# Kernel tuning notes

Measured on AMD Instinct MI355X. Metric: run time of the kernel, lower is better.

Reference implementation:

```python
import jax, jax.numpy as jnp
import numpy as np

B, H, W, C, NH, WS, SS = 32, 56, 56, 192, 6, 7, 3
L = H * W
N = WS * WS
HD = C // NH
EPS = 1e-3  # keras LayerNormalization default epsilon


def _rel_index(ws):
    coords = np.stack(np.meshgrid(np.arange(ws), np.arange(ws), indexing='ij')).reshape(2, -1)
    rel = (coords[:, :, None] - coords[:, None, :]).transpose(1, 2, 0)
    rel[..., 0] += ws - 1
    rel[..., 1] += ws - 1
    rel[..., 0] *= 2 * ws - 1
    return rel.sum(-1)  # (N, N) int


def _attn_mask(h, w, ws, ss):
    img = np.zeros((h, w), np.float32)
    cnt = 0
    for hs in (slice(0, -ws), slice(-ws, -ss), slice(-ss, None)):
        for wsl in (slice(0, -ws), slice(-ws, -ss), slice(-ss, None)):
            img[hs, wsl] = cnt
            cnt += 1
    mw = img.reshape(h // ws, ws, w // ws, ws).transpose(0, 2, 1, 3).reshape(-1, ws * ws)
    diff = mw[:, None, :] - mw[:, :, None]  # expand_dims(mw,1) - expand_dims(mw,2)
    return np.where(diff != 0, -100.0, 0.0).astype(np.float32)  # (nW, N, N)


REL_IDX = _rel_index(WS)
ATTN_MASK = _attn_mask(H, W, WS, SS)


def _ln(x, g, b):
    m = x.mean(-1, keepdims=True)
    v = x.var(-1, keepdims=True)
    return (x - m) / jnp.sqrt(v + EPS) * g + b


def setup_inputs() -> dict:
    key = jax.random.key(0)
    ks = jax.random.split(key, 8)
    s = 0.02
    return {
        'x': jax.random.normal(ks[0], (B, L, C), jnp.float32),
        'gamma1': jnp.ones((C,), jnp.float32),
        'beta1': jnp.zeros((C,), jnp.float32),
        'qkv_w': jax.random.normal(ks[1], (C, 3 * C), jnp.float32) * s,
        'qkv_b': jnp.zeros((3 * C,), jnp.float32),
        'proj_w': jax.random.normal(ks[2], (C, C), jnp.float32) * s,
        'proj_b': jnp.zeros((C,), jnp.float32),
        'rel_bias_table': jax.random.normal(ks[3], ((2 * WS - 1) ** 2, NH), jnp.float32) * s,
        'gamma2': jnp.ones((C,), jnp.float32),
        'beta2': jnp.zeros((C,), jnp.float32),
        'fc1_w': jax.random.normal(ks[4], (C, 4 * C), jnp.float32) * s,
        'fc1_b': jnp.zeros((4 * C,), jnp.float32),
        'fc2_w': jax.random.normal(ks[5], (4 * C, C), jnp.float32) * s,
        'fc2_b': jnp.zeros((C,), jnp.float32),
    }


def reference(x, gamma1, beta1, qkv_w, qkv_b, proj_w, proj_b, rel_bias_table,
              gamma2, beta2, fc1_w, fc1_b, fc2_w, fc2_b):
    scale = HD ** -0.5
    shortcut = x
    # norm1 + cyclic shift + window partition
    xn = _ln(x, gamma1, beta1).reshape(B, H, W, C)
    xn = jnp.roll(xn, (-SS, -SS), axis=(1, 2))
    xw = xn.reshape(B, H // WS, WS, W // WS, WS, C).transpose(0, 1, 3, 2, 4, 5).reshape(-1, N, C)
    # window attention
    qkv = (xw @ qkv_w + qkv_b).reshape(-1, N, 3, NH, HD).transpose(2, 0, 3, 1, 4)
    q, k, v = qkv[0] * scale, qkv[1], qkv[2]  # (B*nW, NH, N, HD)
    attn = jnp.einsum('whnd,whmd->whnm', q, k)
    bias = rel_bias_table[REL_IDX.reshape(-1)].reshape(N, N, NH).transpose(2, 0, 1)
    attn = attn + bias[None]
    nW = ATTN_MASK.shape[0]
    attn = attn.reshape(B, nW, NH, N, N) + jnp.asarray(ATTN_MASK)[None, :, None]
    attn = jax.nn.softmax(attn.reshape(-1, NH, N, N), axis=-1)
    out = jnp.einsum('whnm,whmd->whnd', attn, v).transpose(0, 2, 1, 3).reshape(-1, N, C)
    out = out @ proj_w + proj_b
    # window reverse + reverse shift
    xr = out.reshape(B, H // WS, W // WS, WS, WS, C).transpose(0, 1, 3, 2, 4, 5).reshape(B, H, W, C)
    xr = jnp.roll(xr, (SS, SS), axis=(1, 2)).reshape(B, L, C)
    x = shortcut + xr
    # MLP block
    y = _ln(x, gamma2, beta2)
    y = jax.nn.gelu(y @ fc1_w + fc1_b, approximate=False) @ fc2_w + fc2_b
    return x + y
```

## Files before the change

kernel.cpp:

```cpp
#include <hip/hip_runtime.h>
#include <math.h>

namespace {
constexpr int kBatch = 32, kH = 56, kW = 56, kC = 192, kNH = 6, kWS = 7, kSS = 3;
constexpr int kL   = kH * kW;
constexpr int kN   = kWS * kWS;
constexpr int kTok = kBatch * kL;
constexpr int kNWin = kTok / kN;
constexpr float kEps   = 1e-3f;
constexpr float kScale = 0.17677669529663687f;
}

typedef unsigned short u16;
typedef __attribute__((ext_vector_type(8))) short short8;
typedef __attribute__((ext_vector_type(4))) float f32x4;

__device__ __forceinline__ float bf2f(u16 u) {
    return __uint_as_float(((unsigned int)u) << 16);
}
__device__ __forceinline__ u16 f2bf(float f) {
    unsigned int x = __float_as_uint(f);
    return (u16)((x + 0x7FFFu + ((x >> 16) & 1u)) >> 16);
}
__device__ __forceinline__ float gelu_f(float x) {
    float z = 0.7978845608028654f * x * (1.0f + 0.044715f * x * x);
    float t = 1.0f - 2.0f / (1.0f + __expf(2.0f * z));
    return 0.5f * x * (1.0f + t);
}

__global__ __launch_bounds__(256) void ln_kernel(
    const float* __restrict__ x, const float* __restrict__ gamma,
    const float* __restrict__ beta, u16* __restrict__ out, int do_shift)
{
    const int wave = threadIdx.x >> 6;
    const int lane = threadIdx.x & 63;
    const int tok = (blockIdx.x << 2) + wave;
    const float* xp = x + (size_t)tok * kC;
    float v0 = xp[lane], v1 = xp[lane + 64], v2 = xp[lane + 128];
    float s  = v0 + v1 + v2;
    float sq = v0 * v0 + v1 * v1 + v2 * v2;
    #pragma unroll
    for (int off = 32; off > 0; off >>= 1) {
        s  += __shfl_down(s, off, 64);
        sq += __shfl_down(sq, off, 64);
    }
    s  = __shfl(s, 0, 64);
    sq = __shfl(sq, 0, 64);
    const float mean = s * (1.0f / kC);
    const float var  = sq * (1.0f / kC) - mean * mean;
    const float inv  = rsqrtf(var + kEps);
    size_t orow;
    if (do_shift) {
        const int b = tok / kL, hw = tok % kL;
        const int h = hw / kW, w = hw % kW;
        const int hs = (h + kH - kSS) % kH;
        const int ws = (w + kW - kSS) % kW;
        const int wh = hs / kWS, ii = hs % kWS;
        const int ww = ws / kWS, jj = ws % kWS;
        orow = (size_t)(b * 64 + wh * 8 + ww) * kN + (ii * kWS + jj);
    } else {
        orow = tok;
    }
    u16* op = out + orow * kC;
    op[lane]       = f2bf((v0 - mean) * inv * gamma[lane]       + beta[lane]);
    op[lane + 64]  = f2bf((v1 - mean) * inv * gamma[lane + 64]  + beta[lane + 64]);
    op[lane + 128] = f2bf((v2 - mean) * inv * gamma[lane + 128] + beta[lane + 128]);
}

__global__ __launch_bounds__(256) void wprep_qkv(
    const float* __restrict__ w, u16* __restrict__ wt)
{
    const int idx = blockIdx.x * 256 + threadIdx.x;
    if (idx >= 576 * 192) return;
    const int n = idx / 192, k = idx - n * 192;
    float v = w[(size_t)k * 576 + n];
    if (n < 192) v *= kScale;
    wt[idx] = f2bf(v);
}

__global__ __launch_bounds__(256) void wprep_rest(
    const float* __restrict__ pw, const float* __restrict__ f1w,
    const float* __restrict__ f2w, u16* __restrict__ proj_t,
    u16* __restrict__ f1_t, u16* __restrict__ f2_t)
{
    int idx = blockIdx.x * 256 + threadIdx.x;
    if (idx < 36864) {
        const int n = idx / 192, k = idx - n * 192;
        proj_t[idx] = f2bf(pw[(size_t)k * 192 + n]);
        return;
    }
    idx -= 36864;
    if (idx < 147456) {
        const int n = idx / 192, k = idx - n * 192;
        f1_t[idx] = f2bf(f1w[(size_t)k * 768 + n]);
        return;
    }
    idx -= 147456;
    if (idx < 147456) {
        const int n = idx / 768, k = idx - n * 768;
        f2_t[idx] = f2bf(f2w[(size_t)k * 192 + n]);
    }
}

__global__ __launch_bounds__(256) void prep_bm(
    const float* __restrict__ btab, const float* __restrict__ qkv_b,
    float* __restrict__ T, float* __restrict__ qkv_bs)
{
    const int idx = blockIdx.x * 256 + threadIdx.x;
    if (idx < 576) qkv_bs[idx] = (idx < 192) ? qkv_b[idx] * kScale : qkv_b[idx];
    if (idx >= 4 * 6 * 49 * 49) return;
    const int m = idx % 49, n = (idx / 49) % 49;
    const int head = (idx / 2401) % 6, cls = idx / (2401 * 6);
    const int i1 = n / 7, j1 = n % 7, i2 = m / 7, j2 = m % 7;
    float v = btab[((i1 - i2 + 6) * 13 + (j1 - j2 + 6)) * kNH + head];
    const int whE = cls >> 1, wwE = cls & 1;
    const int r1 = (whE ? (i1 < 4 ? 1 : 2) : 0) * 3 + (wwE ? (j1 < 4 ? 1 : 2) : 0);
    const int r2 = (whE ? (i2 < 4 ? 1 : 2) : 0) * 3 + (wwE ? (j2 < 4 ? 1 : 2) : 0);
    if (r1 != r2) v -= 100.f;
    T[idx] = v;
}

template <int MODE, int K, int NJ>
__global__ __launch_bounds__(256) void gemm_mfma(
    const u16* __restrict__ A, const u16* __restrict__ Bt, int ldb,
    const float* __restrict__ bias, const float* __restrict__ aux,
    void* __restrict__ outv, u16* __restrict__ vt = nullptr)
{
    constexpr int Nn = NJ * 192;
    constexpr int Kp = K + 8;
    __shared__ u16 As[64 * Kp];
    const int tid  = threadIdx.x;
    const int wave = tid >> 6, lane = tid & 63;
    const int quad = lane >> 4, l15 = lane & 15;
    const int m0 = blockIdx.x * 64;

    {
        const u16* src = A + (size_t)m0 * K;
        #pragma unroll
        for (int i = tid; i < 64 * K / 8; i += 256) {
            const int e = i * 8;
            const int r = e / K, c = e - r * K;
            *(short8*)&As[r * Kp + c] = *(const short8*)(src + e);
        }
    }
    __syncthreads();

    #pragma unroll
    for (int j = 0; j < NJ; ++j) {
        const int nb0 = j * 192 + wave * 48;
        const u16* Bbase = Bt + (size_t)(nb0 + l15) * ldb + quad * 8;
        f32x4 acc[4][3] = {};
        #pragma unroll
        for (int ks = 0; ks < K / 32; ++ks) {
            short8 a[4], b[3];
            #pragma unroll
            for (int i = 0; i < 4; ++i)
                a[i] = *(const short8*)&As[(i * 16 + l15) * Kp + ks * 32 + quad * 8];
            #pragma unroll
            for (int t = 0; t < 3; ++t)
                b[t] = *(const short8*)(Bbase + (size_t)t * 16 * ldb + ks * 32);
            #pragma unroll
            for (int i = 0; i < 4; ++i)
                #pragma unroll
                for (int t = 0; t < 3; ++t)
                    acc[i][t] = __builtin_amdgcn_mfma_f32_16x16x32_bf16(
                        a[i], b[t], acc[i][t], 0, 0, 0);
        }
        float bcol[3] = {0.f, 0.f, 0.f};
        {
            #pragma unroll
            for (int t = 0; t < 3; ++t) bcol[t] = bias[nb0 + t * 16 + l15];
        }
        #pragma unroll
        for (int i = 0; i < 4; ++i) {
            #pragma unroll
            for (int reg = 0; reg < 4; ++reg) {
                const int r = m0 + i * 16 + quad * 4 + reg;
                if (MODE == 2) {
                    const int win = r / kN, n = r % kN;
                    const int b = win >> 6, wi = win & 63;
                    const int wh = wi >> 3, ww = wi & 7;
                    const int i1 = n / kWS, j1 = n % kWS;
                    const int h = (wh * kWS + i1 + kSS) % kH;
                    const int w = (ww * kWS + j1 + kSS) % kW;
                    const size_t drow = ((size_t)b * kL + h * kW + w) * kC;
                    #pragma unroll
                    for (int t = 0; t < 3; ++t) {
                        const int c = nb0 + t * 16 + l15;
                        const size_t dest = drow + c;
                        ((float*)outv)[dest] = acc[i][t][reg] + bcol[t] + aux[dest];
                    }
                } else if (MODE == 5 && j == 2) {
                    const int win = r / kN, n = r - win * kN;
                    #pragma unroll
                    for (int t = 0; t < 3; ++t) {
                        const int d = nb0 - 384 + t * 16 + l15;
                        const size_t off =
                            ((size_t)win * 192 + d) * 64 + n;
                        vt[off] = f2bf(acc[i][t][reg] + bcol[t]);
                    }
                } else {
                    #pragma unroll
                    for (int t = 0; t < 3; ++t) {
                        const int c = nb0 + t * 16 + l15;
                        float v = acc[i][t][reg] + bcol[t];
                        ((u16*)outv)[(size_t)r * Nn + c] = f2bf(v);
                    }
                }
            }
        }
    }
}

__global__ __launch_bounds__(256, 2) void mlp_fused(
    float* __restrict__ out,
    const float* __restrict__ gamma, const float* __restrict__ beta,
    const u16* __restrict__ f1_t, const float* __restrict__ fc1_b,
    const u16* __restrict__ f2_t, const float* __restrict__ fc2_b)
{
    constexpr int Kp = 200;
    constexpr int Kh = 392;
    __shared__ u16 As[64 * Kp];
    __shared__ u16 Hs[64 * Kh];
    const int tid  = threadIdx.x;
    const int wave = tid >> 6, lane = tid & 63;
    const int quad = lane >> 4, l15 = lane & 15;
    const int m0 = blockIdx.x * 64;

    for (int it = 0; it < 16; ++it) {
        const int r = it * 4 + wave;
        const float* xp = out + (size_t)(m0 + r) * kC;
        float v0 = xp[lane], v1 = xp[lane + 64], v2 = xp[lane + 128];
        float s  = v0 + v1 + v2;
        float sq = v0 * v0 + v1 * v1 + v2 * v2;
        #pragma unroll
        for (int off = 32; off > 0; off >>= 1) {
            s  += __shfl_down(s, off, 64);
            sq += __shfl_down(sq, off, 64);
        }
        s  = __shfl(s, 0, 64);
        sq = __shfl(sq, 0, 64);
        const float mean = s * (1.0f / kC);
        const float inv  = rsqrtf(sq * (1.0f / kC) - mean * mean + kEps);
        As[r * Kp + lane]       = f2bf((v0 - mean) * inv * gamma[lane]       + beta[lane]);
        As[r * Kp + lane + 64]  = f2bf((v1 - mean) * inv * gamma[lane + 64]  + beta[lane + 64]);
        As[r * Kp + lane + 128] = f2bf((v2 - mean) * inv * gamma[lane + 128] + beta[lane + 128]);
    }
    __syncthreads();

    f32x4 acc2[4][3] = {};
    #pragma unroll
    for (int h = 0; h < 2; ++h) {
        f32x4 acc1[4][6] = {};
        const u16* B1 = f1_t + (size_t)(h * 384 + wave * 96 + l15) * 192 + quad * 8;
        #pragma unroll
        for (int ks = 0; ks < 6; ++ks) {
            short8 a[4], b[6];
            #pragma unroll
            for (int i = 0; i < 4; ++i)
                a[i] = *(const short8*)&As[(i * 16 + l15) * Kp + ks * 32 + quad * 8];
            #pragma unroll
            for (int t = 0; t < 6; ++t)
                b[t] = *(const short8*)(B1 + (size_t)t * 16 * 192 + ks * 32);
            #pragma unroll
            for (int i = 0; i < 4; ++i)
                #pragma unroll
                for (int t = 0; t < 6; ++t)
                    acc1[i][t] = __builtin_amdgcn_mfma_f32_16x16x32_bf16(
                        a[i], b[t], acc1[i][t], 0, 0, 0);
        }
        __syncthreads();
        #pragma unroll
        for (int t = 0; t < 6; ++t) {
            const int c  = wave * 96 + t * 16 + l15;
            const float bb = fc1_b[h * 384 + c];
            #pragma unroll
            for (int i = 0; i < 4; ++i) {
                #pragma unroll
                for (int reg = 0; reg < 4; ++reg) {
                    const int r = i * 16 + quad * 4 + reg;
                    Hs[r * Kh + c] = f2bf(gelu_f(acc1[i][t][reg] + bb));
                }
            }
        }
        __syncthreads();
        const u16* B2 = f2_t + (size_t)(wave * 48 + l15) * 768 + h * 384 + quad * 8;
        #pragma unroll
        for (int ks = 0; ks < 12; ++ks) {
            short8 a[4], b[3];
            #pragma unroll
            for (int i = 0; i < 4; ++i)
                a[i] = *(const short8*)&Hs[(i * 16 + l15) * Kh + ks * 32 + quad * 8];
            #pragma unroll
            for (int t = 0; t < 3; ++t)
                b[t] = *(const short8*)(B2 + (size_t)t * 16 * 768 + ks * 32);
            #pragma unroll
            for (int i = 0; i < 4; ++i)
                #pragma unroll
                for (int t = 0; t < 3; ++t)
                    acc2[i][t] = __builtin_amdgcn_mfma_f32_16x16x32_bf16(
                        a[i], b[t], acc2[i][t], 0, 0, 0);
        }
    }
    #pragma unroll
    for (int t = 0; t < 3; ++t) {
        const int c  = wave * 48 + t * 16 + l15;
        const float bb = fc2_b[c];
        #pragma unroll
        for (int i = 0; i < 4; ++i) {
            #pragma unroll
            for (int reg = 0; reg < 4; ++reg) {
                const int r = m0 + i * 16 + quad * 4 + reg;
                float* p = out + (size_t)r * kC + c;
                *p = acc2[i][t][reg] + bb + *p;
            }
        }
    }
}

__global__ __launch_bounds__(256) void attn_mfma(
    const u16* __restrict__ qkv, const u16* __restrict__ vt,
    const float* __restrict__ T, u16* __restrict__ out)
{
    __shared__ u16 Ps[4][64][72];
    const int tid = threadIdx.x;
    const int wave = tid >> 6, lane = tid & 63;
    const int quad = lane >> 4, l15 = lane & 15;
    const int pair = blockIdx.x * 4 + wave;
    const int win = pair / 6, head = pair - win * 6;
    const int wi = win & 63;
    const int cls = (((wi >> 3) == 7) ? 2 : 0) + (((wi & 7) == 7) ? 1 : 0);
    const float* Tb = T + (size_t)(cls * 6 + head) * 49 * 49;

    const u16* base = qkv + (size_t)win * 49 * 576 + head * 32 + quad * 8;
    short8 zz = {};
    short8 qa[4], kb[4];
    #pragma unroll
    for (int i = 0; i < 4; ++i) {
        const int n = i * 16 + l15;
        qa[i] = (n < 49) ? *(const short8*)(base + (size_t)n * 576) : zz;
        kb[i] = (n < 49) ? *(const short8*)(base + (size_t)n * 576 + 192) : zz;
    }
    f32x4 acc[4][4];
    #pragma unroll
    for (int i = 0; i < 4; ++i) {
        #pragma unroll
        for (int reg = 0; reg < 4; ++reg) {
            const int n = i * 16 + quad * 4 + reg;
            const bool nv = (n < 49);
            const float* Trow = Tb + (nv ? n : 0) * 49;
            #pragma unroll
            for (int j = 0; j < 3; ++j)
                acc[i][j][reg] = nv ? Trow[j * 16 + l15] : 0.f;
            acc[i][3][reg] = (nv && l15 == 0) ? Trow[48] : -30000.f;
        }
    }
    #pragma unroll
    for (int i = 0; i < 4; ++i)
        #pragma unroll
        for (int j = 0; j < 4; ++j)
            acc[i][j] = __builtin_amdgcn_mfma_f32_16x16x32_bf16(
                qa[i], kb[j], acc[i][j], 0, 0, 0);
    float rowinv[4][4];
    #pragma unroll
    for (int i = 0; i < 4; ++i) {
        #pragma unroll
        for (int reg = 0; reg < 4; ++reg) {
            const int n = i * 16 + quad * 4 + reg;
            float e0 = __expf(acc[i][0][reg]), e1 = __expf(acc[i][1][reg]);
            float e2 = __expf(acc[i][2][reg]), e3 = __expf(acc[i][3][reg]);
            float sum = e0 + e1 + e2 + e3;
            #pragma unroll
            for (int off = 1; off < 16; off <<= 1)
                sum += __shfl_xor(sum, off, 64);
            rowinv[i][reg] = 1.0f / sum;
            Ps[wave][n][0 * 16 + l15] = f2bf(e0);
            Ps[wave][n][1 * 16 + l15] = f2bf(e1);
            Ps[wave][n][2 * 16 + l15] = f2bf(e2);
            Ps[wave][n][3 * 16 + l15] = f2bf(e3);
        }
    }
    const u16* vb_base = vt + ((size_t)pair * 32 + l15) * 64 + quad * 8;
    f32x4 o[4][2] = {};
    #pragma unroll
    for (int ks = 0; ks < 2; ++ks) {
        short8 pa[4], vb[2];
        #pragma unroll
        for (int i = 0; i < 4; ++i)
            pa[i] = *(const short8*)&Ps[wave][i * 16 + l15][ks * 32 + quad * 8];
        #pragma unroll
        for (int t = 0; t < 2; ++t)
            vb[t] = *(const short8*)(vb_base + (size_t)t * 16 * 64 + ks * 32);
        #pragma unroll
        for (int i = 0; i < 4; ++i)
            #pragma unroll
            for (int t = 0; t < 2; ++t)
                o[i][t] = __builtin_amdgcn_mfma_f32_16x16x32_bf16(
                    pa[i], vb[t], o[i][t], 0, 0, 0);
    }
    u16* obase = out + (size_t)win * 49 * 192 + head * 32;
    #pragma unroll
    for (int i = 0; i < 4; ++i) {
        #pragma unroll
        for (int reg = 0; reg < 4; ++reg) {
            const int n = i * 16 + quad * 4 + reg;
            if (n < 49) {
                const float inv = rowinv[i][reg];
                obase[(size_t)n * 192 + l15]      = f2bf(o[i][0][reg] * inv);
                obase[(size_t)n * 192 + 16 + l15] = f2bf(o[i][1][reg] * inv);
            }
        }
    }
}

extern "C" void kernel_launch(void* const* d_in, const int* in_sizes, int n_in,
                              void* d_out, int out_size, void* d_ws, size_t ws_size,
                              hipStream_t stream)
{
    const float* x      = (const float*)d_in[0];
    const float* gamma1 = (const float*)d_in[1];
    const float* beta1  = (const float*)d_in[2];
    const float* qkv_w  = (const float*)d_in[3];
    const float* qkv_b  = (const float*)d_in[4];
    const float* proj_w = (const float*)d_in[5];
    const float* proj_b = (const float*)d_in[6];
    const float* btab   = (const float*)d_in[7];
    const float* gamma2 = (const float*)d_in[8];
    const float* beta2  = (const float*)d_in[9];
    const float* fc1_w  = (const float*)d_in[10];
    const float* fc1_b  = (const float*)d_in[11];
    const float* fc2_w  = (const float*)d_in[12];
    const float* fc2_b  = (const float*)d_in[13];
    float* out = (float*)d_out;

    u16* buf_a = (u16*)d_ws;
    u16* buf_b = buf_a + (size_t)kTok * 192;
    u16* qkv_t = (u16*)d_out;
    float* bm_tab = (float*)d_out + 55296;
    float* qkv_bs = bm_tab + 57624;
    u16* vT = (u16*)d_out + 230400;
    u16* wt2   = (u16*)d_ws + (size_t)kTok * 768 - 331776;
    u16* proj_t = wt2;
    u16* f1_t   = wt2 + 36864;
    u16* f2_t   = f1_t + 147456;

    wprep_qkv<<<(110592 + 255) / 256, 256, 0, stream>>>(qkv_w, qkv_t);
    prep_bm<<<(57624 + 255) / 256, 256, 0, stream>>>(btab, qkv_b, bm_tab, qkv_bs);
    ln_kernel<<<kTok / 4, 256, 0, stream>>>(x, gamma1, beta1, buf_a, 1);
    gemm_mfma<5, 192, 3><<<kTok / 64, 256, 0, stream>>>(
        buf_a, qkv_t, 192, qkv_bs, nullptr, buf_b, vT);
    attn_mfma<<<(kNWin * kNH) / 4, 256, 0, stream>>>(buf_b, vT, bm_tab, buf_a);
    wprep_rest<<<(331776 + 255) / 256, 256, 0, stream>>>(
        proj_w, fc1_w, fc2_w, proj_t, f1_t, f2_t);
    gemm_mfma<2, 192, 1><<<kTok / 64, 256, 0, stream>>>(
        buf_a, proj_t, 192, proj_b, x, out);
    mlp_fused<<<kTok / 64, 256, 0, stream>>>(
        out, gamma2, beta2, f1_t, fc1_b, f2_t, fc2_b);
}
```

Measured before the change: 577.4 us.

## Split fused MLP block across 8 waves and vectorize its LayerNorm prologue

The fused MLP kernel now launches 512 threads (8 waves) per 64-row tile instead of 4 waves. Waves are arranged 2x4 so each handles 32 rows instead of 64, which halves per-wave accumulator registers and aims for more waves in flight per CU. The LayerNorm prologue now has 16 lanes per row using float4 loads and packed bf16 stores, with gamma/beta held in registers. In exchange, each B-fragment of the weights is loaded twice per block (once per row half), which raises global/L2 traffic. Shared memory per block is unchanged, so the higher occupancy requested by the launch bounds may not be reached.

After: 646.3 us. 11.9% more time.

```diff
diff --git a/kernel.cpp b/kernel.cpp
--- a/kernel.cpp
+++ b/kernel.cpp
@@ -212,7 +212,7 @@
     }
 }
 
-__global__ __launch_bounds__(256, 2) void mlp_fused(
+__global__ __launch_bounds__(512, 4) void mlp_fused(
     float* __restrict__ out,
     const float* __restrict__ gamma, const float* __restrict__ beta,
     const u16* __restrict__ f1_t, const float* __restrict__ fc1_b,
@@ -225,45 +225,62 @@
     const int tid  = threadIdx.x;
     const int wave = tid >> 6, lane = tid & 63;
     const int quad = lane >> 4, l15 = lane & 15;
+    const int wm = wave >> 2, wn = wave & 3;
     const int m0 = blockIdx.x * 64;
 
-    for (int it = 0; it < 16; ++it) {
-        const int r = it * 4 + wave;
-        const float* xp = out + (size_t)(m0 + r) * kC;
-        float v0 = xp[lane], v1 = xp[lane + 64], v2 = xp[lane + 128];
-        float s  = v0 + v1 + v2;
-        float sq = v0 * v0 + v1 * v1 + v2 * v2;
-        #pragma unroll
-        for (int off = 32; off > 0; off >>= 1) {
-            s  += __shfl_down(s, off, 64);
-            sq += __shfl_down(sq, off, 64);
-        }
-        s  = __shfl(s, 0, 64);
-        sq = __shfl(sq, 0, 64);
-        const float mean = s * (1.0f / kC);
-        const float inv  = rsqrtf(sq * (1.0f / kC) - mean * mean + kEps);
-        As[r * Kp + lane]       = f2bf((v0 - mean) * inv * gamma[lane]       + beta[lane]);
-        As[r * Kp + lane + 64]  = f2bf((v1 - mean) * inv * gamma[lane + 64]  + beta[lane + 64]);
-        As[r * Kp + lane + 128] = f2bf((v2 - mean) * inv * gamma[lane + 128] + beta[lane + 128]);
+    {
+        float gv[12], bv[12];
+        #pragma unroll
+        for (int j = 0; j < 12; ++j) {
+            gv[j] = gamma[l15 * 12 + j];
+            bv[j] = beta[l15 * 12 + j];
+        }
+        #pragma unroll
+        for (int it = 0; it < 2; ++it) {
+            const int r = it * 32 + wave * 4 + quad;
+            const float* xp = out + (size_t)(m0 + r) * kC + l15 * 12;
+            float4 u0 = *(const float4*)(xp);
+            float4 u1 = *(const float4*)(xp + 4);
+            float4 u2 = *(const float4*)(xp + 8);
+            float v[12] = {u0.x, u0.y, u0.z, u0.w, u1.x, u1.y, u1.z, u1.w,
+                           u2.x, u2.y, u2.z, u2.w};
+            float s = 0.f, sq = 0.f;
+            #pragma unroll
+            for (int j = 0; j < 12; ++j) { s += v[j]; sq += v[j] * v[j]; }
+            #pragma unroll
+            for (int off = 1; off < 16; off <<= 1) {
+                s  += __shfl_xor(s, off, 64);
+                sq += __shfl_xor(sq, off, 64);
+            }
+            const float mean = s * (1.0f / kC);
+            const float inv  = rsqrtf(sq * (1.0f / kC) - mean * mean + kEps);
+            unsigned* ap = (unsigned*)&As[r * Kp + l15 * 12];
+            #pragma unroll
+            for (int j = 0; j < 6; ++j) {
+                float a0 = (v[2 * j]     - mean) * inv * gv[2 * j]     + bv[2 * j];
+                float a1 = (v[2 * j + 1] - mean) * inv * gv[2 * j + 1] + bv[2 * j + 1];
+                ap[j] = (unsigned)f2bf(a0) | ((unsigned)f2bf(a1) << 16);
+            }
+        }
     }
     __syncthreads();
 
-    f32x4 acc2[4][3] = {};
+    f32x4 acc2[2][3] = {};
     #pragma unroll
     for (int h = 0; h < 2; ++h) {
-        f32x4 acc1[4][6] = {};
-        const u16* B1 = f1_t + (size_t)(h * 384 + wave * 96 + l15) * 192 + quad * 8;
+        f32x4 acc1[2][6] = {};
+        const u16* B1 = f1_t + (size_t)(h * 384 + wn * 96 + l15) * 192 + quad * 8;
         #pragma unroll
         for (int ks = 0; ks < 6; ++ks) {
-            short8 a[4], b[6];
-            #pragma unroll
-            for (int i = 0; i < 4; ++i)
-                a[i] = *(const short8*)&As[(i * 16 + l15) * Kp + ks * 32 + quad * 8];
+            short8 a[2], b[6];
+            #pragma unroll
+            for (int i = 0; i < 2; ++i)
+                a[i] = *(const short8*)&As[(wm * 32 + i * 16 + l15) * Kp + ks * 32 + quad * 8];
             #pragma unroll
             for (int t = 0; t < 6; ++t)
                 b[t] = *(const short8*)(B1 + (size_t)t * 16 * 192 + ks * 32);
             #pragma unroll
-            for (int i = 0; i < 4; ++i)
+            for (int i = 0; i < 2; ++i)
                 #pragma unroll
                 for (int t = 0; t < 6; ++t)
                     acc1[i][t] = __builtin_amdgcn_mfma_f32_16x16x32_bf16(
@@ -272,30 +289,30 @@
         __syncthreads();
         #pragma unroll
         for (int t = 0; t < 6; ++t) {
-            const int c  = wave * 96 + t * 16 + l15;
+            const int c  = wn * 96 + t * 16 + l15;
             const float bb = fc1_b[h * 384 + c];
             #pragma unroll
-            for (int i = 0; i < 4; ++i) {
+            for (int i = 0; i < 2; ++i) {
                 #pragma unroll
                 for (int reg = 0; reg < 4; ++reg) {
-                    const int r = i * 16 + quad * 4 + reg;
+                    const int r = wm * 32 + i * 16 + quad * 4 + reg;
                     Hs[r * Kh + c] = f2bf(gelu_f(acc1[i][t][reg] + bb));
                 }
             }
         }
         __syncthreads();
-        const u16* B2 = f2_t + (size_t)(wave * 48 + l15) * 768 + h * 384 + quad * 8;
+        const u16* B2 = f2_t + (size_t)(wn * 48 + l15) * 768 + h * 384 + quad * 8;
         #pragma unroll
         for (int ks = 0; ks < 12; ++ks) {
-            short8 a[4], b[3];
-            #pragma unroll
-            for (int i = 0; i < 4; ++i)
-                a[i] = *(const short8*)&Hs[(i * 16 + l15) * Kh + ks * 32 + quad * 8];
+            short8 a[2], b[3];
+            #pragma unroll
+            for (int i = 0; i < 2; ++i)
+                a[i] = *(const short8*)&Hs[(wm * 32 + i * 16 + l15) * Kh + ks * 32 + quad * 8];
             #pragma unroll
             for (int t = 0; t < 3; ++t)
                 b[t] = *(const short8*)(B2 + (size_t)t * 16 * 768 + ks * 32);
             #pragma unroll
-            for (int i = 0; i < 4; ++i)
+            for (int i = 0; i < 2; ++i)
                 #pragma unroll
                 for (int t = 0; t < 3; ++t)
                     acc2[i][t] = __builtin_amdgcn_mfma_f32_16x16x32_bf16(
@@ -304,13 +321,13 @@
     }
     #pragma unroll
     for (int t = 0; t < 3; ++t) {
-        const int c  = wave * 48 + t * 16 + l15;
+        const int c  = wn * 48 + t * 16 + l15;
         const float bb = fc2_b[c];
         #pragma unroll
-        for (int i = 0; i < 4; ++i) {
+        for (int i = 0; i < 2; ++i) {
             #pragma unroll
             for (int reg = 0; reg < 4; ++reg) {
-                const int r = m0 + i * 16 + quad * 4 + reg;
+                const int r = m0 + wm * 32 + i * 16 + quad * 4 + reg;
                 float* p = out + (size_t)r * kC + c;
                 *p = acc2[i][t][reg] + bb + *p;
             }
@@ -454,6 +471,6 @@
         proj_w, fc1_w, fc2_w, proj_t, f1_t, f2_t);
     gemm_mfma<2, 192, 1><<<kTok / 64, 256, 0, stream>>>(
         buf_a, proj_t, 192, proj_b, x, out);
-    mlp_fused<<<kTok / 64, 256, 0, stream>>>(
+    mlp_fused<<<kTok / 64, 512, 0, stream>>>(
         out, gamma2, beta2, f1_t, fc1_b, f2_t, fc2_b);
 }
```
